# Kernel tuning notes

Measured on AMD Instinct MI355X. Metric: run time of the kernel, lower is better.

Reference implementation:

```python
import jax, jax.numpy as jnp
import numpy as np

B, S, E, H = 4, 2048, 1024, 16
Dh = E // H
EPS = 1e-5


def setup_inputs() -> dict:
    key = jax.random.key(0)
    ks = jax.random.split(key, 16)
    w = lambda k, shp: jax.random.normal(k, shp, dtype=jnp.float32) * 0.02
    return {
        "x": jax.random.normal(ks[0], (B, S, E), dtype=jnp.float32),
        "Wq": w(ks[1], (E, E)), "bq": jnp.zeros((E,), jnp.float32),
        "Wk": w(ks[2], (E, E)), "bk": jnp.zeros((E,), jnp.float32),
        "Wv": w(ks[3], (E, E)), "bv": jnp.zeros((E,), jnp.float32),
        "Wo": w(ks[4], (E, E)), "bo": jnp.zeros((E,), jnp.float32),
        "an1_a": jnp.ones((1, S, 1), jnp.float32),
        "an1_b": jnp.zeros((1, S, 1), jnp.float32),
        "W1": w(ks[5], (2 * E, E)), "b1": jnp.zeros((2 * E,), jnp.float32),
        "W2": w(ks[6], (E, 2 * E)), "b2": jnp.zeros((E,), jnp.float32),
        "an2_a": jnp.ones((1, S, 1), jnp.float32),
        "an2_b": jnp.zeros((1, S, 1), jnp.float32),
    }


def adaptive_norm(x, a, b):
    # AdaptiveNorm((1, N_s, 1)): normalize over embedding dim, per-position affine.
    mu = jnp.mean(x, axis=-1, keepdims=True)
    var = jnp.mean(jnp.square(x - mu), axis=-1, keepdims=True)
    return a * (x - mu) * jax.lax.rsqrt(var + EPS) + b


def reference(x, Wq, bq, Wk, bk, Wv, bv, Wo, bo, an1_a, an1_b, W1, b1, W2, b2, an2_a, an2_b):
    scale = 1.0 / np.sqrt(E / H)
    # QKV projections -> (B, S, H, Dh)
    q = (x @ Wq.T + bq).reshape(B, S, H, Dh)
    k = (x @ Wk.T + bk).reshape(B, S, H, Dh)
    v = (x @ Wv.T + bv).reshape(B, S, H, Dh)
    # scaled dot-product attention (materializes B,H,S,S like the original)
    scores = jnp.einsum("bshd,bthd->bhst", q, k) * scale
    probs = jax.nn.softmax(scores, axis=-1)
    attn = jnp.einsum("bhst,bthd->bshd", probs, v).reshape(B, S, E)
    attn = attn @ Wo.T + bo
    # residual + adaptive norm (dropout is identity in eval mode)
    h = adaptive_norm(attn + x, an1_a, an1_b)
    ff = jax.nn.relu(h @ W1.T + b1) @ W2.T + b2
    out = adaptive_norm(ff + h, an2_a, an2_b)
    return out
```

## Files before the change

kernel.cpp:

```cpp
#include <hip/hip_runtime.h>


typedef __attribute__((ext_vector_type(8))) short s16x8;
typedef __attribute__((ext_vector_type(4))) short s16x4;
typedef __attribute__((ext_vector_type(4))) unsigned short u16x4;
typedef __attribute__((ext_vector_type(4))) float f32x4;

__device__ __forceinline__ float bf2f(unsigned short u) {
  unsigned int v = ((unsigned int)u) << 16;
  return __builtin_bit_cast(float, v);
}
__device__ __forceinline__ unsigned short f2bf(float f) {
  unsigned int u = __builtin_bit_cast(unsigned int, f);
  u += 0x7fffu + ((u >> 16) & 1u);
  return (unsigned short)(u >> 16);
}
__device__ __forceinline__ unsigned int pkbf_trunc(float f0, float f1) {
  return __builtin_amdgcn_perm(__builtin_bit_cast(unsigned int, f1),
                               __builtin_bit_cast(unsigned int, f0), 0x07060302u);
}
__device__ __forceinline__ f32x4 mfma16(s16x8 a, s16x8 b, f32x4 c) {
  return __builtin_amdgcn_mfma_f32_16x16x32_bf16(a, b, c, 0, 0, 0);
}
__device__ __forceinline__ void gl2lds16(const unsigned short* g, unsigned short* l) {
  __builtin_amdgcn_global_load_lds(
      (const __attribute__((address_space(1))) unsigned int*)(g),
      (__attribute__((address_space(3))) unsigned int*)(l), 16, 0, 0);
}

__global__ void detect_dtype(const unsigned int* __restrict__ x, int* __restrict__ flag) {
  const int tid = threadIdx.x;
  int cnt = 0;
  for (int i = tid; i < 2048; i += 256) {
    const unsigned e = (x[i] >> 7) & 0xFF;
    cnt += (e >= 100 && e <= 150) ? 1 : 0;
  }
#pragma unroll
  for (int off = 32; off >= 1; off >>= 1) cnt += __shfl_xor(cnt, off);
  __shared__ int red[4];
  if ((tid & 63) == 0) red[tid >> 6] = cnt;
  __syncthreads();
  if (tid == 0) *flag = ((red[0] + red[1] + red[2] + red[3]) > 1536) ? 1 : 0;
}

struct CvtArgs {
  const void* src[17];
  unsigned short* dst[17];
  int cum4[18];
};

__global__ __launch_bounds__(256) void cvt_all(CvtArgs a, const int* __restrict__ flag, int total4) {
  const int i = blockIdx.x * 256 + threadIdx.x;
  if (i >= total4) return;
  int lo = 0, hi = 17;
  while (hi - lo > 1) {
    const int mid = (lo + hi) >> 1;
    if (i >= a.cum4[mid]) lo = mid; else hi = mid;
  }
  const int off4 = i - a.cum4[lo];
  if (*flag) {
    const u16x4* s = (const u16x4*)a.src[lo];
    *(u16x4*)&a.dst[lo][off4 * 4] = s[off4];
  } else {
    const float4* s = (const float4*)a.src[lo];
    const float4 v = s[off4];
    u16x4 o;
    o[0] = f2bf(v.x); o[1] = f2bf(v.y); o[2] = f2bf(v.z); o[3] = f2bf(v.w);
    *(u16x4*)&a.dst[lo][off4 * 4] = o;
  }
}

#define BM 128
#define BN 128
#define BKK 64
#define QOFF 8388608L
#define SCALE2 0.18033688011f

template <int EPI>
__global__ __launch_bounds__(256, 2) void gemm_bt(
    const unsigned short* __restrict__ A, const unsigned short* __restrict__ W,
    const unsigned short* __restrict__ bias, const unsigned short* __restrict__ resid,
    unsigned short* __restrict__ out, int M, int N, int K) {
  __shared__ unsigned short Al[BM * BKK];
  __shared__ unsigned short Bl[BN * BKK];
  const int tid = threadIdx.x;
  const int lane = tid & 63;
  const int wave = tid >> 6;
  const int qd = lane >> 4;
  const int c = lane & 15;
  const int wm = (wave >> 1) * 64;
  const int wn = (wave & 1) * 64;
  const long m0 = (long)blockIdx.y * BM;
  const long n0 = (long)blockIdx.x * BN;

  f32x4 acc[4][4] = {};

  const int scc = ((tid & 7) ^ ((tid >> 3) & 7)) * 8;
  const unsigned short* Ag = A + (m0 + (tid >> 3)) * (long)K + scc;
  const unsigned short* Wg = W + (n0 + (tid >> 3)) * (long)K + scc;

  for (int k0 = 0; k0 < K; k0 += BKK) {
    __syncthreads();
#pragma unroll
    for (int p = 0; p < 4; ++p)
      gl2lds16(Ag + (long)p * 32 * K + k0, &Al[(p * 256 + tid) * 8]);
#pragma unroll
    for (int p = 0; p < 4; ++p)
      gl2lds16(Wg + (long)p * 32 * K + k0, &Bl[(p * 256 + tid) * 8]);
    __syncthreads();
#pragma unroll
    for (int ks = 0; ks < 2; ++ks) {
      const int ch = ((ks * 4 + qd) ^ (c & 7)) * 8;
      s16x8 af[4], bfr[4];
#pragma unroll
      for (int mt = 0; mt < 4; ++mt)
        af[mt] = *(const s16x8*)&Al[(wm + mt * 16 + c) * BKK + ch];
#pragma unroll
      for (int nt = 0; nt < 4; ++nt)
        bfr[nt] = *(const s16x8*)&Bl[(wn + nt * 16 + c) * BKK + ch];
#pragma unroll
      for (int mt = 0; mt < 4; ++mt)
#pragma unroll
        for (int nt = 0; nt < 4; ++nt)
          acc[mt][nt] = mfma16(af[mt], bfr[nt], acc[mt][nt]);
    }
  }

#pragma unroll
  for (int nt = 0; nt < 4; ++nt) {
    const int gn = (int)n0 + wn + nt * 16 + c;
    const float bv = bf2f(bias[gn]);
#pragma unroll
    for (int mt = 0; mt < 4; ++mt) {
      const long gmb = m0 + wm + mt * 16 + qd * 4;
      if constexpr (EPI == 2) {
#pragma unroll
        for (int r = 0; r < 4; ++r) {
          const long gm = gmb + r;
          const float v = acc[mt][nt][r] + bv + bf2f(resid[gm * N + gn]);
          out[gm * N + gn] = f2bf(v);
        }
      } else if constexpr (EPI == 3) {
#pragma unroll
        for (int r = 0; r < 4; ++r) {
          const long gm = gmb + r;
          float v = acc[mt][nt][r] + bv;
          v = fmaxf(v, 0.0f);
          out[gm * N + gn] = f2bf(v);
        }
      } else {
        const int seg = gn >> 10;
        const int nn = gn & 1023;
        const int h = nn >> 6, d = nn & 63;
        if (seg == 0) {
#pragma unroll
          for (int r = 0; r < 4; ++r) {
            const long gm = gmb + r;
            const long b = gm >> 11;
            const int s = (int)(gm & 2047);
            out[((b * 16 + h) * 2048L + s) * 64 + d] =
                f2bf((acc[mt][nt][r] + bv) * SCALE2);
          }
        } else if (seg == 1) {
#pragma unroll
          for (int r = 0; r < 4; ++r) {
            const long gm = gmb + r;
            const long b = gm >> 11;
            const int s = (int)(gm & 2047);
            (out + QOFF)[((b * 16 + h) * 2048L + s) * 64 + d] =
                f2bf(acc[mt][nt][r] + bv);
          }
        } else {
          const long b = gmb >> 11;
          const int s = (int)(gmb & 2047);
          s16x4 pv;
#pragma unroll
          for (int r = 0; r < 4; ++r) pv[r] = (short)f2bf(acc[mt][nt][r] + bv);
          *(s16x4*)&(out + 2 * QOFF)[((b * 16 + h) * 64L + d) * 2048 + s] = pv;
        }
      }
    }
  }
}

#define ATT_S 2048

__global__ __launch_bounds__(256, 2) void attn_fwd(
    const unsigned short* __restrict__ Q, const unsigned short* __restrict__ K,
    const unsigned short* __restrict__ VT, unsigned short* __restrict__ O) {
  __shared__ unsigned short SH[128 * 136 + 64 * 128];
  unsigned short* Kl = SH;
  unsigned short* Pl = SH;
  unsigned short* VTl = SH + 128 * 136;

  const int bh = blockIdx.y;
  const int q0 = blockIdx.x * 128;
  const unsigned short* Qh = Q + (long)bh * ATT_S * 64;
  const unsigned short* Kg = K + (long)bh * ATT_S * 64;
  const unsigned short* Vg = VT + (long)bh * 64 * ATT_S;

  const int tid = threadIdx.x;
  const int wave = tid >> 6, lane = tid & 63;
  const int qd = lane >> 4, c = lane & 15;
  const int mb = wave * 32;

  s16x8 qf[2][2];
#pragma unroll
  for (int mt = 0; mt < 2; ++mt)
#pragma unroll
    for (int ks = 0; ks < 2; ++ks)
      qf[mt][ks] = *(const s16x8*)&Qh[(long)(q0 + mb + mt * 16 + c) * 64 + ks * 32 + qd * 8];

  s16x8 ones;
#pragma unroll
  for (int i = 0; i < 8; ++i) ones[i] = (short)0x3F80;

  f32x4 oacc[4][2] = {};
  f32x4 lacc[2] = {};

  const int kscc = ((tid & 7) ^ ((tid >> 3) & 7)) * 8;
  const int vscc = ((tid & 15) ^ ((tid >> 4) & 15)) * 8;

  for (int kv = 0; kv < ATT_S; kv += 128) {
    __syncthreads();
#pragma unroll
    for (int p = 0; p < 4; ++p) {
      const int idx = p * 256 + tid;
      gl2lds16(Kg + (long)kv * 64 + (long)(idx >> 3) * 64 + kscc, &Kl[idx * 8]);
    }
#pragma unroll
    for (int p = 0; p < 4; ++p) {
      const int idx = p * 256 + tid;
      gl2lds16(Vg + (long)(idx >> 4) * ATT_S + kv + vscc,
               &VTl[(idx >> 4) * 128 + (idx & 15) * 8]);
    }
    __syncthreads();

    f32x4 sacc[8][2] = {};
#pragma unroll
    for (int ks = 0; ks < 2; ++ks) {
      const int ch = ((ks * 4 + qd) ^ (c & 7)) * 8;
      s16x8 kf[8];
#pragma unroll
      for (int tt = 0; tt < 8; ++tt)
        kf[tt] = *(const s16x8*)&Kl[(tt * 16 + c) * 64 + ch];
#pragma unroll
      for (int mt = 0; mt < 2; ++mt)
#pragma unroll
        for (int tt = 0; tt < 8; ++tt)
          sacc[tt][mt] = mfma16(kf[tt], qf[mt][ks], sacc[tt][mt]);
    }

    __syncthreads();

#pragma unroll
    for (int mt = 0; mt < 2; ++mt) {
      const int ml = mb + mt * 16 + c;
#pragma unroll
      for (int tt = 0; tt < 8; ++tt) {
        unsigned int pk[2];
        pk[0] = pkbf_trunc(exp2f(sacc[tt][mt][0]), exp2f(sacc[tt][mt][1]));
        pk[1] = pkbf_trunc(exp2f(sacc[tt][mt][2]), exp2f(sacc[tt][mt][3]));
        *(uint2*)&Pl[ml * 136 + tt * 16 + qd * 4] = *(uint2*)pk;
      }
    }
    asm volatile("s_waitcnt lgkmcnt(0)" ::: "memory");

#pragma unroll
    for (int ks = 0; ks < 4; ++ks) {
      const int vch = ((ks * 4 + qd) ^ c) * 8;
      s16x8 vf[4], pf[2];
#pragma unroll
      for (int dt = 0; dt < 4; ++dt)
        vf[dt] = *(const s16x8*)&VTl[(dt * 16 + c) * 128 + vch];
#pragma unroll
      for (int mt = 0; mt < 2; ++mt)
        pf[mt] = *(const s16x8*)&Pl[(mb + mt * 16 + c) * 136 + ks * 32 + qd * 8];
#pragma unroll
      for (int mt = 0; mt < 2; ++mt) {
#pragma unroll
        for (int dt = 0; dt < 4; ++dt)
          oacc[dt][mt] = mfma16(vf[dt], pf[mt], oacc[dt][mt]);
        lacc[mt] = mfma16(ones, pf[mt], lacc[mt]);
      }
    }
  }

  const long b = bh >> 4;
  const int h = bh & 15;
#pragma unroll
  for (int mt = 0; mt < 2; ++mt) {
    const float inv = 1.0f / lacc[mt][0];
    const int s = q0 + mb + mt * 16 + c;
    const long ob = (b * (long)ATT_S + s) * 1024L + h * 64;
#pragma unroll
    for (int dt = 0; dt < 4; ++dt) {
      s16x4 ov;
#pragma unroll
      for (int r = 0; r < 4; ++r) ov[r] = (short)f2bf(oacc[dt][mt][r] * inv);
      *(s16x4*)&O[ob + dt * 16 + qd * 4] = ov;
    }
  }
}

template <bool FINAL>
__global__ __launch_bounds__(256) void norm_affine(
    const unsigned short* __restrict__ X, const unsigned short* __restrict__ av,
    const unsigned short* __restrict__ bv, void* __restrict__ outv,
    const int* __restrict__ flag) {
  const int row = blockIdx.x;
  const int s = row & 2047;
  const unsigned short* xr = X + (long)row * 1024;
  const int tid = threadIdx.x;
  const u16x4 u = *(const u16x4*)&xr[tid * 4];
  float v[4];
  float s1 = 0.f, s2 = 0.f;
#pragma unroll
  for (int i = 0; i < 4; ++i) {
    v[i] = bf2f(u[i]);
    s1 += v[i];
    s2 += v[i] * v[i];
  }
#pragma unroll
  for (int off = 32; off >= 1; off >>= 1) {
    s1 += __shfl_xor(s1, off);
    s2 += __shfl_xor(s2, off);
  }
  __shared__ float red[8];
  const int wave = tid >> 6, lane = tid & 63;
  if (lane == 0) {
    red[wave * 2] = s1;
    red[wave * 2 + 1] = s2;
  }
  __syncthreads();
  s1 = red[0] + red[2] + red[4] + red[6];
  s2 = red[1] + red[3] + red[5] + red[7];
  const float mean = s1 * (1.0f / 1024.0f);
  const float var = fmaxf(s2 * (1.0f / 1024.0f) - mean * mean, 0.0f);
  const float rstd = rsqrtf(var + 1e-5f);
  const float aa = bf2f(av[s]), bb = bf2f(bv[s]);
  float o[4];
#pragma unroll
  for (int i = 0; i < 4; ++i) o[i] = aa * (v[i] - mean) * rstd + bb;
  bool as_bf16 = true;
  if constexpr (FINAL) as_bf16 = (*flag != 0);
  if (as_bf16) {
    u16x4 ob;
#pragma unroll
    for (int i = 0; i < 4; ++i) ob[i] = f2bf(o[i]);
    *(u16x4*)&((unsigned short*)outv)[(long)row * 1024 + tid * 4] = ob;
  } else {
    float4 of = {o[0], o[1], o[2], o[3]};
    *(float4*)&((float*)outv)[(long)row * 1024 + tid * 4] = of;
  }
}

extern "C" void kernel_launch(void* const* d_in, const int* in_sizes, int n_in,
                              void* d_out, int out_size, void* d_ws, size_t ws_size,
                              hipStream_t stream) {
  char* ws = (char*)d_ws;
  const size_t SZ = 8192ull * 1024 * 2;
  const size_t WSZ = 1024ull * 1024 * 2;

  unsigned short* xb   = (unsigned short*)(ws);
  unsigned short* qb   = (unsigned short*)(ws + SZ);
  unsigned short* kb   = (unsigned short*)(ws + 2 * SZ);
  unsigned short* vtb  = (unsigned short*)(ws + 3 * SZ);
  unsigned short* attn = (unsigned short*)(ws + 4 * SZ);
  unsigned short* hb   = (unsigned short*)(ws + 5 * SZ);
  unsigned short* r1   = qb;
  unsigned short* ffb  = kb;
  unsigned short* r2   = attn;

  char* wreg = ws + 6 * SZ;
  unsigned short* wqb = (unsigned short*)(wreg);
  unsigned short* w1b = (unsigned short*)(wreg + 4 * WSZ);
  unsigned short* w2b = (unsigned short*)(wreg + 6 * WSZ);
  unsigned short* wob = (unsigned short*)(wreg + 3 * WSZ);
  unsigned short* smal = (unsigned short*)(wreg + 8 * WSZ);
  unsigned short* bqb = smal;
  unsigned short* bkb = smal + 1024;
  unsigned short* bvb = smal + 2048;
  unsigned short* bob = smal + 3072;
  unsigned short* b1b = smal + 4096;
  unsigned short* b2b = smal + 6144;
  unsigned short* a1b = smal + 7168;
  unsigned short* g1b = smal + 9216;
  unsigned short* a2b = smal + 11264;
  unsigned short* g2b = smal + 13312;
  int* flag = (int*)(wreg + 8 * WSZ + 64 * 1024);

  CvtArgs ca;
  unsigned short* wkb = wqb + 1024 * 1024;
  unsigned short* wvb = wqb + 2 * 1024 * 1024;
  unsigned short* dsts[17] = {xb, wqb, bqb, wkb, bkb, wvb, bvb, wob, bob,
                              a1b, g1b, w1b, b1b, w2b, b2b, a2b, g2b};
  ca.cum4[0] = 0;
  for (int i = 0; i < 17; ++i) {
    ca.src[i] = d_in[i];
    ca.dst[i] = dsts[i];
    ca.cum4[i + 1] = ca.cum4[i] + in_sizes[i] / 4;
  }
  const int total4 = ca.cum4[17];

  dim3 blk(256);
  detect_dtype<<<1, blk, 0, stream>>>((const unsigned int*)d_in[0], flag);
  cvt_all<<<(total4 + 255) / 256, blk, 0, stream>>>(ca, flag, total4);

  gemm_bt<4><<<dim3(24, 64), blk, 0, stream>>>(xb, wqb, bqb, nullptr, qb, 8192, 3072, 1024);
  attn_fwd<<<dim3(16, 64), blk, 0, stream>>>(qb, kb, vtb, attn);
  gemm_bt<2><<<dim3(8, 64), blk, 0, stream>>>(attn, wob, bob, xb, r1, 8192, 1024, 1024);
  norm_affine<false><<<8192, blk, 0, stream>>>(r1, a1b, g1b, hb, nullptr);
  gemm_bt<3><<<dim3(16, 64), blk, 0, stream>>>(hb, w1b, b1b, nullptr, ffb, 8192, 2048, 1024);
  gemm_bt<2><<<dim3(8, 64), blk, 0, stream>>>(ffb, w2b, b2b, hb, r2, 8192, 1024, 2048);
  norm_affine<true><<<8192, blk, 0, stream>>>(r2, a2b, g2b, d_out, flag);
}
```

Before: 478.0 us.

## Process two query tiles per attention block to reuse K/V tiles

Each attention block now handles 256 query rows, split into two halves of 128, and reuses every K and V tile loaded into LDS for both halves. This halves the K/V global traffic and the number of sync rounds per query row. P moves to its own LDS region with an XOR-swizzled layout instead of aliasing K, which removes one barrier. The cost is a larger LDS footprint (64 KB), more registers for the two accumulator sets, and half as many blocks, which can reduce occupancy and parallelism across the GPU.

```diff
diff --git a/kernel.cpp b/kernel.cpp
--- a/kernel.cpp
+++ b/kernel.cpp
@@ -188,13 +188,13 @@
 __global__ __launch_bounds__(256, 2) void attn_fwd(
     const unsigned short* __restrict__ Q, const unsigned short* __restrict__ K,
     const unsigned short* __restrict__ VT, unsigned short* __restrict__ O) {
-  __shared__ unsigned short SH[128 * 136 + 64 * 128];
+  __shared__ unsigned short SH[32768];
   unsigned short* Kl = SH;
-  unsigned short* Pl = SH;
-  unsigned short* VTl = SH + 128 * 136;
+  unsigned short* VTl = SH + 128 * 64;
+  unsigned short* Pl = SH + 128 * 64 + 64 * 128;
 
   const int bh = blockIdx.y;
-  const int q0 = blockIdx.x * 128;
+  const int q0 = blockIdx.x * 256;
   const unsigned short* Qh = Q + (long)bh * ATT_S * 64;
   const unsigned short* Kg = K + (long)bh * ATT_S * 64;
   const unsigned short* Vg = VT + (long)bh * 64 * ATT_S;
@@ -204,19 +204,22 @@
   const int qd = lane >> 4, c = lane & 15;
   const int mb = wave * 32;
 
-  s16x8 qf[2][2];
-#pragma unroll
-  for (int mt = 0; mt < 2; ++mt)
-#pragma unroll
-    for (int ks = 0; ks < 2; ++ks)
-      qf[mt][ks] = *(const s16x8*)&Qh[(long)(q0 + mb + mt * 16 + c) * 64 + ks * 32 + qd * 8];
+  s16x8 qf[2][2][2];
+#pragma unroll
+  for (int h2 = 0; h2 < 2; ++h2)
+#pragma unroll
+    for (int mt = 0; mt < 2; ++mt)
+#pragma unroll
+      for (int ks = 0; ks < 2; ++ks)
+        qf[h2][mt][ks] = *(const s16x8*)&Qh[(long)(q0 + h2 * 128 + mb + mt * 16 + c) * 64 +
+                                            ks * 32 + qd * 8];
 
   s16x8 ones;
 #pragma unroll
   for (int i = 0; i < 8; ++i) ones[i] = (short)0x3F80;
 
-  f32x4 oacc[4][2] = {};
-  f32x4 lacc[2] = {};
+  f32x4 oacc[2][4][2] = {};
+  f32x4 lacc[2][2] = {};
 
   const int kscc = ((tid & 7) ^ ((tid >> 3) & 7)) * 8;
   const int vscc = ((tid & 15) ^ ((tid >> 4) & 15)) * 8;
@@ -236,52 +239,56 @@
     }
     __syncthreads();
 
-    f32x4 sacc[8][2] = {};
-#pragma unroll
-    for (int ks = 0; ks < 2; ++ks) {
-      const int ch = ((ks * 4 + qd) ^ (c & 7)) * 8;
-      s16x8 kf[8];
-#pragma unroll
-      for (int tt = 0; tt < 8; ++tt)
-        kf[tt] = *(const s16x8*)&Kl[(tt * 16 + c) * 64 + ch];
-#pragma unroll
-      for (int mt = 0; mt < 2; ++mt)
+#pragma unroll
+    for (int h2 = 0; h2 < 2; ++h2) {
+      f32x4 sacc[8][2] = {};
+#pragma unroll
+      for (int ks = 0; ks < 2; ++ks) {
+        const int ch = ((ks * 4 + qd) ^ (c & 7)) * 8;
+        s16x8 kf[8];
 #pragma unroll
         for (int tt = 0; tt < 8; ++tt)
-          sacc[tt][mt] = mfma16(kf[tt], qf[mt][ks], sacc[tt][mt]);
-    }
-
-    __syncthreads();
-
-#pragma unroll
-    for (int mt = 0; mt < 2; ++mt) {
-      const int ml = mb + mt * 16 + c;
-#pragma unroll
-      for (int tt = 0; tt < 8; ++tt) {
-        unsigned int pk[2];
-        pk[0] = pkbf_trunc(exp2f(sacc[tt][mt][0]), exp2f(sacc[tt][mt][1]));
-        pk[1] = pkbf_trunc(exp2f(sacc[tt][mt][2]), exp2f(sacc[tt][mt][3]));
-        *(uint2*)&Pl[ml * 136 + tt * 16 + qd * 4] = *(uint2*)pk;
+          kf[tt] = *(const s16x8*)&Kl[(tt * 16 + c) * 64 + ch];
+#pragma unroll
+        for (int mt = 0; mt < 2; ++mt)
+#pragma unroll
+          for (int tt = 0; tt < 8; ++tt)
+            sacc[tt][mt] = mfma16(kf[tt], qf[h2][mt][ks], sacc[tt][mt]);
       }
-    }
-    asm volatile("s_waitcnt lgkmcnt(0)" ::: "memory");
-
-#pragma unroll
-    for (int ks = 0; ks < 4; ++ks) {
-      const int vch = ((ks * 4 + qd) ^ c) * 8;
-      s16x8 vf[4], pf[2];
-#pragma unroll
-      for (int dt = 0; dt < 4; ++dt)
-        vf[dt] = *(const s16x8*)&VTl[(dt * 16 + c) * 128 + vch];
-#pragma unroll
-      for (int mt = 0; mt < 2; ++mt)
-        pf[mt] = *(const s16x8*)&Pl[(mb + mt * 16 + c) * 136 + ks * 32 + qd * 8];
+
 #pragma unroll
       for (int mt = 0; mt < 2; ++mt) {
+        const int ml = mb + mt * 16 + c;
+#pragma unroll
+        for (int tt = 0; tt < 8; ++tt) {
+          unsigned int pk[2];
+          pk[0] = pkbf_trunc(exp2f(sacc[tt][mt][0]), exp2f(sacc[tt][mt][1]));
+          pk[1] = pkbf_trunc(exp2f(sacc[tt][mt][2]), exp2f(sacc[tt][mt][3]));
+          const int chw = ((tt * 2 + (qd >> 1)) ^ (ml & 7)) * 8 + (qd & 1) * 4;
+          *(uint2*)&Pl[ml * 128 + chw] = *(uint2*)pk;
+        }
+      }
+      asm volatile("s_waitcnt lgkmcnt(0)" ::: "memory");
+
+#pragma unroll
+      for (int ks = 0; ks < 4; ++ks) {
+        const int vch = ((ks * 4 + qd) ^ c) * 8;
+        s16x8 vf[4], pf[2];
 #pragma unroll
         for (int dt = 0; dt < 4; ++dt)
-          oacc[dt][mt] = mfma16(vf[dt], pf[mt], oacc[dt][mt]);
-        lacc[mt] = mfma16(ones, pf[mt], lacc[mt]);
+          vf[dt] = *(const s16x8*)&VTl[(dt * 16 + c) * 128 + vch];
+#pragma unroll
+        for (int mt = 0; mt < 2; ++mt) {
+          const int pr = mb + mt * 16 + c;
+          pf[mt] = *(const s16x8*)&Pl[pr * 128 + (((ks * 4 + qd) ^ (pr & 7)) * 8)];
+        }
+#pragma unroll
+        for (int mt = 0; mt < 2; ++mt) {
+#pragma unroll
+          for (int dt = 0; dt < 4; ++dt)
+            oacc[h2][dt][mt] = mfma16(vf[dt], pf[mt], oacc[h2][dt][mt]);
+          lacc[h2][mt] = mfma16(ones, pf[mt], lacc[h2][mt]);
+        }
       }
     }
   }
@@ -289,18 +296,20 @@
   const long b = bh >> 4;
   const int h = bh & 15;
 #pragma unroll
-  for (int mt = 0; mt < 2; ++mt) {
-    const float inv = 1.0f / lacc[mt][0];
-    const int s = q0 + mb + mt * 16 + c;
-    const long ob = (b * (long)ATT_S + s) * 1024L + h * 64;
-#pragma unroll
-    for (int dt = 0; dt < 4; ++dt) {
-      s16x4 ov;
-#pragma unroll
-      for (int r = 0; r < 4; ++r) ov[r] = (short)f2bf(oacc[dt][mt][r] * inv);
-      *(s16x4*)&O[ob + dt * 16 + qd * 4] = ov;
-    }
-  }
+  for (int h2 = 0; h2 < 2; ++h2)
+#pragma unroll
+    for (int mt = 0; mt < 2; ++mt) {
+      const float inv = 1.0f / lacc[h2][mt][0];
+      const int s = q0 + h2 * 128 + mb + mt * 16 + c;
+      const long ob = (b * (long)ATT_S + s) * 1024L + h * 64;
+#pragma unroll
+      for (int dt = 0; dt < 4; ++dt) {
+        s16x4 ov;
+#pragma unroll
+        for (int r = 0; r < 4; ++r) ov[r] = (short)f2bf(oacc[h2][dt][mt][r] * inv);
+        *(s16x4*)&O[ob + dt * 16 + qd * 4] = ov;
+      }
+    }
 }
 
 template <bool FINAL>
@@ -408,7 +417,7 @@
   cvt_all<<<(total4 + 255) / 256, blk, 0, stream>>>(ca, flag, total4);
 
   gemm_bt<4><<<dim3(24, 64), blk, 0, stream>>>(xb, wqb, bqb, nullptr, qb, 8192, 3072, 1024);
-  attn_fwd<<<dim3(16, 64), blk, 0, stream>>>(qb, kb, vtb, attn);
+  attn_fwd<<<dim3(8, 64), blk, 0, stream>>>(qb, kb, vtb, attn);
   gemm_bt<2><<<dim3(8, 64), blk, 0, stream>>>(attn, wob, bob, xb, r1, 8192, 1024, 1024);
   norm_affine<false><<<8192, blk, 0, stream>>>(r1, a1b, g1b, hb, nullptr);
   gemm_bt<3><<<dim3(16, 64), blk, 0, stream>>>(hb, w1b, b1b, nullptr, ffb, 8192, 2048, 1024);
```

Result: faster. 459.6 us (-3.9%).
